# Performance work log

Hardware: AMD Instinct MI355X
Metric: run time of the kernel (lower is better)

The kernel has to match this reference:

```python
import jax, jax.numpy as jnp
import numpy as np

GAMMA = 0.99
EPS = 1e-8
N = 16777216  # flattened reward count


def setup_inputs() -> dict:
    key = jax.random.key(0)
    rewards = jax.random.normal(key, (N,), dtype=jnp.float32)
    return {"rewards": rewards}


def reference(rewards):
    # Sequential recurrence: R_t = gamma*R_{t-1} + r_t, Welford stats over R_t,
    # scaled[i] = r_i / max(std_t, eps), std_t = sqrt(var_sum/count) (1.0 if count < 2).
    flat = rewards.reshape(-1)

    def step(carry, r):
        R, cnt, mean, var_sum = carry
        R = GAMMA * R + r
        cnt = cnt + 1.0
        delta = R - mean
        mean = mean + delta / cnt
        var_sum = var_sum + delta * (R - mean)
        std = jnp.where(cnt < 2.0, jnp.float32(1.0), jnp.sqrt(var_sum / cnt))
        std = jnp.maximum(std, jnp.float32(EPS))
        return (R, cnt, mean, var_sum), r / std

    init = (jnp.float32(0.0), jnp.float32(0.0), jnp.float32(0.0), jnp.float32(0.0))
    _, scaled = jax.lax.scan(step, init, flat)
    return scaled.reshape(rewards.shape)
```

## Files before the change

### kernel.cpp

```cpp
#include <hip/hip_runtime.h>
#include <math.h>

#define THREADS 256
#define GAMMA 0.99

typedef float vf4 __attribute__((ext_vector_type(4)));

__device__ __forceinline__ int padi16(int i) { return i + (i >> 4); }

template<int NW>
__device__ __forceinline__ void block_compose_excl(int tid, double g, double v,
                                                   double& eg, double& ev,
                                                   double* lg, double* lv) {
    const int lane = tid & 63, wave = tid >> 6;
    double ig = g, iv = v;
#pragma unroll
    for (int k = 1; k < 64; k <<= 1) {
        double og = __shfl_up(ig, k);
        double ov = __shfl_up(iv, k);
        if (lane >= k) { iv = fma(ig, ov, iv); ig *= og; }
    }
    double weg = __shfl_up(ig, 1);
    double wev = __shfl_up(iv, 1);
    if (lane == 0) { weg = 1.0; wev = 0.0; }
    if (lane == 63) { lg[wave] = ig; lv[wave] = iv; }
    __syncthreads();
    double bg = 1.0, bv = 0.0;
    for (int w = 0; w < wave; ++w) { bv = fma(lg[w], bv, lv[w]); bg *= lg[w]; }
    eg = weg * bg;
    ev = fma(weg, bv, wev);
}

template<int NW>
__device__ __forceinline__ void block_add_excl2(int tid, double a, double b,
                                                double& ea, double& eb,
                                                double* la, double* lb) {
    const int lane = tid & 63, wave = tid >> 6;
    double ia = a, ib = b;
#pragma unroll
    for (int k = 1; k < 64; k <<= 1) {
        double oa = __shfl_up(ia, k);
        double ob = __shfl_up(ib, k);
        if (lane >= k) { ia += oa; ib += ob; }
    }
    double wea = __shfl_up(ia, 1);
    double web = __shfl_up(ib, 1);
    if (lane == 0) { wea = 0.0; web = 0.0; }
    if (lane == 63) { la[wave] = ia; lb[wave] = ib; }
    __syncthreads();
    double ba = 0.0, bb = 0.0;
    for (int w = 0; w < wave; ++w) { ba += la[w]; bb += lb[w]; }
    ea = wea + ba;
    eb = web + bb;
}


__global__ __launch_bounds__(THREADS) void w_phase1(const float* __restrict__ in,
                                                    double* __restrict__ agg,
                                                    double* __restrict__ bagg, int nw) {
    __shared__ double sA[4], sPs[4], sPq[4], sP2[4];
    const int tid = threadIdx.x, lane = tid & 63, w = tid >> 6;
    const int wid = blockIdx.x * 4 + w;
    const bool valid = wid < nw;

    float A = 0.f, c1 = 0.f, c2 = 0.f, c3 = 0.f;
    if (valid) {
        const float* src = in + (size_t)wid * 1024 + (size_t)lane * 16;
        float rv[16];
#pragma unroll
        for (int q = 0; q < 4; ++q) {
            const float4 t = ((const float4*)src)[q];
            rv[4 * q] = t.x; rv[4 * q + 1] = t.y; rv[4 * q + 2] = t.z; rv[4 * q + 3] = t.w;
        }
        const float gf = (float)GAMMA;
        float p = 0.f, psum = 0.f, pq = 0.f, p2 = 0.f, gp = 1.f;
#pragma unroll
        for (int j = 0; j < 16; ++j) {
            p = fmaf(gf, p, rv[j]);
            gp *= gf;
            psum += p;
            pq = fmaf(gp, p, pq);
            p2 = fmaf(p, p, p2);
        }
        const double g = GAMMA;
        double gPT = g;
#pragma unroll
        for (int e = 0; e < 4; ++e) gPT *= gPT;

        float ig = (float)gPT, iv = p;
#pragma unroll
        for (int k = 1; k < 64; k <<= 1) {
            float og = __shfl_up(ig, k);
            float ov = __shfl_up(iv, k);
            if (lane >= k) { iv = fmaf(ig, ov, iv); ig *= og; }
        }
        float rho = __shfl_up(iv, 1), gexc = __shfl_up(ig, 1);
        if (lane == 0) { rho = 0.f; gexc = 1.f; }
        A = __shfl(iv, 63);

        const float G1f = (float)(g * (1.0 - gPT) / (1.0 - g));
        const float G2f = (float)(g * g * (1.0 - gPT * gPT) / (1.0 - g * g));
        c1 = fmaf(rho, G1f, psum);
        c2 = gexc * fmaf(rho, G2f, pq);
        c3 = fmaf(rho * rho, G2f, fmaf(2.f * rho, pq, p2));
#pragma unroll
        for (int k = 32; k > 0; k >>= 1) {
            c1 += __shfl_down(c1, k);
            c2 += __shfl_down(c2, k);
            c3 += __shfl_down(c3, k);
        }
    }
    if (lane == 0) {
        if (valid) {
            agg[4 * (size_t)wid + 0] = (double)A;
            agg[4 * (size_t)wid + 1] = (double)c1;
            agg[4 * (size_t)wid + 2] = (double)c2;
            agg[4 * (size_t)wid + 3] = (double)c3;
        }
        sA[w] = valid ? (double)A : 0.0;
        sPs[w] = valid ? (double)c1 : 0.0;
        sPq[w] = valid ? (double)c2 : 0.0;
        sP2[w] = valid ? (double)c3 : 0.0;
    }
    __syncthreads();
    if (tid == 0) {
        const double g = GAMMA;
        double gC = g;
#pragma unroll
        for (int e = 0; e < 10; ++e) gC *= gC;
        const double G1C = g * (1.0 - gC) / (1.0 - g);
        const double G2C = g * g * (1.0 - gC * gC) / (1.0 - g * g);
        double Rin = 0.0, Ps = 0.0, Pq = 0.0, P2 = 0.0, gex = 1.0;
#pragma unroll
        for (int i = 0; i < 4; ++i) {
            Ps += fma(Rin, G1C, sPs[i]);
            Pq += gex * fma(Rin, G2C, sPq[i]);
            P2 += fma(Rin * Rin, G2C, fma(2.0 * Rin, sPq[i], sP2[i]));
            Rin = fma(gC, Rin, sA[i]);
            gex *= gC;
        }
        bagg[4 * (size_t)blockIdx.x + 0] = Rin;
        bagg[4 * (size_t)blockIdx.x + 1] = Ps;
        bagg[4 * (size_t)blockIdx.x + 2] = Pq;
        bagg[4 * (size_t)blockIdx.x + 3] = P2;
    }
}

template<int CPT, int LOG2CHUNK>
__global__ __launch_bounds__(1024) void rs_phase2(const double* __restrict__ agg,
                                                  double* __restrict__ car, int nchunk) {
    __shared__ double lg[16], lv[16], la[16], lb[16];
    const int t = threadIdx.x;
    const double g = GAMMA;
    double gC = g;
#pragma unroll
    for (int e = 0; e < LOG2CHUNK; ++e) gC *= gC;

    double A[CPT], Ps[CPT], Pq[CPT], P2[CPT];
    const int c0 = t * CPT;
#pragma unroll
    for (int i = 0; i < CPT; ++i) {
        const int c = c0 + i;
        const bool ok = c < nchunk;
        A[i]  = ok ? agg[4 * (size_t)c + 0] : 0.0;
        Ps[i] = ok ? agg[4 * (size_t)c + 1] : 0.0;
        Pq[i] = ok ? agg[4 * (size_t)c + 2] : 0.0;
        P2[i] = ok ? agg[4 * (size_t)c + 3] : 0.0;
    }
    double mg = 1.0, mv = 0.0;
#pragma unroll
    for (int i = 0; i < CPT; ++i) { mv = fma(gC, mv, A[i]); mg *= gC; }

    double eg, ev;
    block_compose_excl<16>(t, mg, mv, eg, ev, lg, lv);

    const double G1C = g * (1.0 - gC) / (1.0 - g);
    const double G2C = g * g * (1.0 - gC * gC) / (1.0 - g * g);
    double Rin[CPT + 1];
    Rin[0] = ev;
    double s1[CPT], s2[CPT];
#pragma unroll
    for (int i = 0; i < CPT; ++i) {
        s1[i] = fma(Rin[i], G1C, Ps[i]);
        s2[i] = fma(Rin[i] * Rin[i], G2C, fma(2.0 * Rin[i], Pq[i], P2[i]));
        Rin[i + 1] = fma(gC, Rin[i], A[i]);
    }
    double ts1 = 0.0, ts2 = 0.0;
#pragma unroll
    for (int i = 0; i < CPT; ++i) { ts1 += s1[i]; ts2 += s2[i]; }
    double ea, eb;
    block_add_excl2<16>(t, ts1, ts2, ea, eb, la, lb);
#pragma unroll
    for (int i = 0; i < CPT; ++i) {
        const int c = c0 + i;
        if (c < nchunk) {
            car[3 * (size_t)c + 0] = Rin[i];
            car[3 * (size_t)c + 1] = ea;
            car[3 * (size_t)c + 2] = eb;
        }
        ea += s1[i];
        eb += s2[i];
    }
}

__global__ __launch_bounds__(THREADS) void w_phase3(const float* __restrict__ in,
                                                    float* __restrict__ out,
                                                    const double* __restrict__ agg,
                                                    const double* __restrict__ car, int nw) {
    __shared__ float sbuf[THREADS / 64][1024 + 64];
    const int tid = threadIdx.x, lane = tid & 63, w = tid >> 6;
    const int wid = blockIdx.x * 4 + w;
    if (wid >= nw) return;
    const int b = blockIdx.x;

    const double g = GAMMA;
    double gC = g;
#pragma unroll
    for (int e = 0; e < 10; ++e) gC *= gC;
    const double G1C = g * (1.0 - gC) / (1.0 - g);
    const double G2C = g * g * (1.0 - gC * gC) / (1.0 - g * g);

    double RinC = car[3 * (size_t)b + 0];
    double S1C  = car[3 * (size_t)b + 1];
    double S2C  = car[3 * (size_t)b + 2];
    for (int i = 4 * b; i < wid; ++i) {
        const double Ai = agg[4 * (size_t)i + 0];
        const double Ps = agg[4 * (size_t)i + 1];
        const double Pq = agg[4 * (size_t)i + 2];
        const double P2 = agg[4 * (size_t)i + 3];
        S1C += fma(RinC, G1C, Ps);
        S2C += fma(RinC * RinC, G2C, fma(2.0 * RinC, Pq, P2));
        RinC = fma(gC, RinC, Ai);
    }

    const float* src = in + (size_t)wid * 1024 + (size_t)lane * 16;
    float rv[16];
#pragma unroll
    for (int q = 0; q < 4; ++q) {
        const float4 t = ((const float4*)src)[q];
        rv[4 * q] = t.x; rv[4 * q + 1] = t.y; rv[4 * q + 2] = t.z; rv[4 * q + 3] = t.w;
    }
    const float gf = (float)GAMMA;
    float p = 0.f, psum = 0.f, pq = 0.f, p2 = 0.f, gp = 1.f;
#pragma unroll
    for (int j = 0; j < 16; ++j) {
        p = fmaf(gf, p, rv[j]);
        gp *= gf;
        psum += p;
        pq = fmaf(gp, p, pq);
        p2 = fmaf(p, p, p2);
    }
    double gPT = g;
#pragma unroll
    for (int e = 0; e < 4; ++e) gPT *= gPT;

    if (wid == 0) {
        double ig = gPT, iv = (double)p;
#pragma unroll
        for (int k = 1; k < 64; k <<= 1) {
            double og = __shfl_up(ig, k);
            double ov = __shfl_up(iv, k);
            if (lane >= k) { iv = fma(ig, ov, iv); ig *= og; }
        }
        double rho = __shfl_up(iv, 1), gexc = __shfl_up(ig, 1);
        if (lane == 0) { rho = 0.0; gexc = 1.0; }
        const double rin = fma(gexc, RinC, rho);
        const double G1 = g * (1.0 - gPT) / (1.0 - g);
        const double G2 = g * g * (1.0 - gPT * gPT) / (1.0 - g * g);
        double s1 = fma(rin, G1, (double)psum);
        double s2 = fma(rin * rin, G2, fma(2.0 * rin, (double)pq, (double)p2));
        double ia = s1, ib = s2;
#pragma unroll
        for (int k = 1; k < 64; k <<= 1) {
            double oa = __shfl_up(ia, k);
            double ob = __shfl_up(ib, k);
            if (lane >= k) { ia += oa; ib += ob; }
        }
        double ea = __shfl_up(ia, 1), eb = __shfl_up(ib, 1);
        if (lane == 0) { ea = 0.0; eb = 0.0; }
        double R = rin, S1 = S1C + ea, S2 = S2C + eb;
        const int a0 = lane * 17;
        const size_t gbase = (size_t)lane * 16;
        for (int j = 0; j < 16; ++j) {
            const float rf = rv[j];
            R = fma(g, R, (double)rf);
            S1 += R;
            S2 = fma(R, R, S2);
            float ov;
            if (gbase + j == 0) {
                ov = rf;
            } else {
                const double cnt = (double)(gbase + j + 1);
                const double inv = 1.0 / cnt;
                const double mean = S1 * inv;
                double var = fma(S2, inv, -(mean * mean));
                var = var > 0.0 ? var : 0.0;
                double sd = sqrt(var);
                sd = sd > 1e-8 ? sd : 1e-8;
                ov = (float)((double)rf / sd);
            }
            sbuf[w][a0 + j] = ov;
        }
    } else {
        float ig = (float)gPT, iv = p;
#pragma unroll
        for (int k = 1; k < 64; k <<= 1) {
            float og = __shfl_up(ig, k);
            float ov = __shfl_up(iv, k);
            if (lane >= k) { iv = fmaf(ig, ov, iv); ig *= og; }
        }
        float rho = __shfl_up(iv, 1), gexc = __shfl_up(ig, 1);
        if (lane == 0) { rho = 0.f; gexc = 1.f; }
        const float rin = fmaf(gexc, (float)RinC, rho);
        const float G1f = (float)(g * (1.0 - gPT) / (1.0 - g));
        const float G2f = (float)(g * g * (1.0 - gPT * gPT) / (1.0 - g * g));
        float s1 = fmaf(rin, G1f, psum);
        float s2 = fmaf(rin * rin, G2f, fmaf(2.f * rin, pq, p2));
        float ia = s1, ib = s2;
#pragma unroll
        for (int k = 1; k < 64; k <<= 1) {
            float oa = __shfl_up(ia, k);
            float ob = __shfl_up(ib, k);
            if (lane >= k) { ia += oa; ib += ob; }
        }
        float ea = __shfl_up(ia, 1), eb = __shfl_up(ib, 1);
        if (lane == 0) { ea = 0.f; eb = 0.f; }
        const float S1bf = (float)S1C + ea;
        const float S2bf = (float)S2C + eb;

        float R = rin;
        float ls1 = 0.f, ls2 = 0.f;
        const float base_cnt = (float)((size_t)wid * 1024 + (size_t)lane * 16);
        const int a0 = lane * 17;
#pragma unroll
        for (int j = 0; j < 16; ++j) {
            const float rf = rv[j];
            R = fmaf(gf, R, rf);
            ls1 += R;
            ls2 = fmaf(R, R, ls2);
            const float cnt = base_cnt + (float)(j + 1);
            const float S1f = S1bf + ls1;
            const float S2f = S2bf + ls2;
            float t = fmaf(S2f, cnt, -(S1f * S1f));
            t = fmaxf(t, 1e-12f);
            sbuf[w][a0 + j] = rf * cnt * __builtin_amdgcn_rsqf(t);
        }
    }

    asm volatile("s_waitcnt lgkmcnt(0)" ::: "memory");

    float* dst = out + (size_t)wid * 1024;
#pragma unroll
    for (int k = 0; k < 4; ++k) {
        const int i = lane * 4 + k * 256;
        const int pp = padi16(i);
        vf4 v;
        v.x = sbuf[w][pp]; v.y = sbuf[w][pp + 1]; v.z = sbuf[w][pp + 2]; v.w = sbuf[w][pp + 3];
        __builtin_nontemporal_store(v, (vf4*)(dst + i));
    }
}

extern "C" void kernel_launch(void* const* d_in, const int* in_sizes, int n_in,
                              void* d_out, int out_size, void* d_ws, size_t ws_size,
                              hipStream_t stream) {
    (void)n_in; (void)out_size;
    const float* in = (const float*)d_in[0];
    float* out = (float*)d_out;
    double* ws = (double*)d_ws;
    const int n = in_sizes[0];

    const int nw = n >> 10;
    const int nc = (nw + 3) >> 2;
    const size_t need = (size_t)(4 * nw + 7 * nc) * sizeof(double);
    if ((n % 4096) == 0 && nw >= 4 && nc <= 4096 && ws_size >= need) {
        double* agg  = ws;
        double* bagg = ws + 4 * (size_t)nw;
        double* car  = bagg + 4 * (size_t)nc;
        w_phase1<<<nc, THREADS, 0, stream>>>(in, agg, bagg, nw);
        rs_phase2<4, 12><<<1, 1024, 0, stream>>>(bagg, car, nc);
        w_phase3<<<nc, THREADS, 0, stream>>>(in, out, agg, car, nw);
    } else {
        double* agg  = ws;
        double* bagg = ws + 4 * (size_t)nw;
        double* car  = bagg + 4 * (size_t)nc;
        w_phase1<<<nc, THREADS, 0, stream>>>(in, agg, bagg, nw);
        rs_phase2<4, 12><<<1, 1024, 0, stream>>>(bagg, car, nc);
        w_phase3<<<nc, THREADS, 0, stream>>>(in, out, agg, car, nw);
    }
}
```

Measured before the change: 51.30 us.

## Precompute per-wave carries in scan phase and store wave aggregates as float4

Phase 2 now expands each block carry into per-wave carries by walking that block's four wave aggregates. Phase 3 then reads its carry directly instead of each wave re-walking prior waves' double aggregates. Wave aggregates are stored as packed float4 rather than four doubles, which halves that traffic. The cost is extra serial work and strided writes in the single-block phase 2. Bounds checks and the workspace-size check are also dropped, so the code now assumes n is a multiple of 4096.

```diff
diff --git a/kernel.cpp b/kernel.cpp
--- a/kernel.cpp
+++ b/kernel.cpp
@@ -56,75 +56,63 @@
 
 
 __global__ __launch_bounds__(THREADS) void w_phase1(const float* __restrict__ in,
-                                                    double* __restrict__ agg,
+                                                    vf4* __restrict__ aggf,
                                                     double* __restrict__ bagg, int nw) {
     __shared__ double sA[4], sPs[4], sPq[4], sP2[4];
     const int tid = threadIdx.x, lane = tid & 63, w = tid >> 6;
     const int wid = blockIdx.x * 4 + w;
-    const bool valid = wid < nw;
-
-    float A = 0.f, c1 = 0.f, c2 = 0.f, c3 = 0.f;
-    if (valid) {
-        const float* src = in + (size_t)wid * 1024 + (size_t)lane * 16;
-        float rv[16];
-#pragma unroll
-        for (int q = 0; q < 4; ++q) {
-            const float4 t = ((const float4*)src)[q];
-            rv[4 * q] = t.x; rv[4 * q + 1] = t.y; rv[4 * q + 2] = t.z; rv[4 * q + 3] = t.w;
-        }
-        const float gf = (float)GAMMA;
-        float p = 0.f, psum = 0.f, pq = 0.f, p2 = 0.f, gp = 1.f;
-#pragma unroll
-        for (int j = 0; j < 16; ++j) {
-            p = fmaf(gf, p, rv[j]);
-            gp *= gf;
-            psum += p;
-            pq = fmaf(gp, p, pq);
-            p2 = fmaf(p, p, p2);
-        }
-        const double g = GAMMA;
-        double gPT = g;
-#pragma unroll
-        for (int e = 0; e < 4; ++e) gPT *= gPT;
-
-        float ig = (float)gPT, iv = p;
-#pragma unroll
-        for (int k = 1; k < 64; k <<= 1) {
-            float og = __shfl_up(ig, k);
-            float ov = __shfl_up(iv, k);
-            if (lane >= k) { iv = fmaf(ig, ov, iv); ig *= og; }
-        }
-        float rho = __shfl_up(iv, 1), gexc = __shfl_up(ig, 1);
-        if (lane == 0) { rho = 0.f; gexc = 1.f; }
-        A = __shfl(iv, 63);
-
-        const float G1f = (float)(g * (1.0 - gPT) / (1.0 - g));
-        const float G2f = (float)(g * g * (1.0 - gPT * gPT) / (1.0 - g * g));
-        c1 = fmaf(rho, G1f, psum);
-        c2 = gexc * fmaf(rho, G2f, pq);
-        c3 = fmaf(rho * rho, G2f, fmaf(2.f * rho, pq, p2));
-#pragma unroll
-        for (int k = 32; k > 0; k >>= 1) {
-            c1 += __shfl_down(c1, k);
-            c2 += __shfl_down(c2, k);
-            c3 += __shfl_down(c3, k);
-        }
+
+    const float* src = in + (size_t)wid * 1024 + (size_t)lane * 16;
+    float rv[16];
+#pragma unroll
+    for (int q = 0; q < 4; ++q) {
+        const float4 t = ((const float4*)src)[q];
+        rv[4 * q] = t.x; rv[4 * q + 1] = t.y; rv[4 * q + 2] = t.z; rv[4 * q + 3] = t.w;
+    }
+    const float gf = (float)GAMMA;
+    float p = 0.f, psum = 0.f, pq = 0.f, p2 = 0.f, gp = 1.f;
+#pragma unroll
+    for (int j = 0; j < 16; ++j) {
+        p = fmaf(gf, p, rv[j]);
+        gp *= gf;
+        psum += p;
+        pq = fmaf(gp, p, pq);
+        p2 = fmaf(p, p, p2);
+    }
+    const double g = GAMMA;
+    double gPT = g;
+#pragma unroll
+    for (int e = 0; e < 4; ++e) gPT *= gPT;
+
+    float ig = (float)gPT, iv = p;
+#pragma unroll
+    for (int k = 1; k < 64; k <<= 1) {
+        float og = __shfl_up(ig, k);
+        float ov = __shfl_up(iv, k);
+        if (lane >= k) { iv = fmaf(ig, ov, iv); ig *= og; }
+    }
+    float rho = __shfl_up(iv, 1), gexc = __shfl_up(ig, 1);
+    if (lane == 0) { rho = 0.f; gexc = 1.f; }
+    const float A = __shfl(iv, 63);
+
+    const float G1f = (float)(g * (1.0 - gPT) / (1.0 - g));
+    const float G2f = (float)(g * g * (1.0 - gPT * gPT) / (1.0 - g * g));
+    float c1 = fmaf(rho, G1f, psum);
+    float c2 = gexc * fmaf(rho, G2f, pq);
+    float c3 = fmaf(rho * rho, G2f, fmaf(2.f * rho, pq, p2));
+#pragma unroll
+    for (int k = 32; k > 0; k >>= 1) {
+        c1 += __shfl_down(c1, k);
+        c2 += __shfl_down(c2, k);
+        c3 += __shfl_down(c3, k);
     }
     if (lane == 0) {
-        if (valid) {
-            agg[4 * (size_t)wid + 0] = (double)A;
-            agg[4 * (size_t)wid + 1] = (double)c1;
-            agg[4 * (size_t)wid + 2] = (double)c2;
-            agg[4 * (size_t)wid + 3] = (double)c3;
-        }
-        sA[w] = valid ? (double)A : 0.0;
-        sPs[w] = valid ? (double)c1 : 0.0;
-        sPq[w] = valid ? (double)c2 : 0.0;
-        sP2[w] = valid ? (double)c3 : 0.0;
+        vf4 a; a.x = A; a.y = c1; a.z = c2; a.w = c3;
+        aggf[wid] = a;
+        sA[w] = (double)A; sPs[w] = (double)c1; sPq[w] = (double)c2; sP2[w] = (double)c3;
     }
     __syncthreads();
     if (tid == 0) {
-        const double g = GAMMA;
         double gC = g;
 #pragma unroll
         for (int e = 0; e < 10; ++e) gC *= gC;
@@ -147,14 +135,18 @@
 }
 
 template<int CPT, int LOG2CHUNK>
-__global__ __launch_bounds__(1024) void rs_phase2(const double* __restrict__ agg,
-                                                  double* __restrict__ car, int nchunk) {
+__global__ __launch_bounds__(1024) void rs_phase2x(const double* __restrict__ bagg,
+                                                   const vf4* __restrict__ aggf,
+                                                   double* __restrict__ wcar, int nchunk) {
     __shared__ double lg[16], lv[16], la[16], lb[16];
     const int t = threadIdx.x;
     const double g = GAMMA;
     double gC = g;
 #pragma unroll
     for (int e = 0; e < LOG2CHUNK; ++e) gC *= gC;
+    double gW = g;
+#pragma unroll
+    for (int e = 0; e < 10; ++e) gW *= gW;
 
     double A[CPT], Ps[CPT], Pq[CPT], P2[CPT];
     const int c0 = t * CPT;
@@ -162,10 +154,10 @@
     for (int i = 0; i < CPT; ++i) {
         const int c = c0 + i;
         const bool ok = c < nchunk;
-        A[i]  = ok ? agg[4 * (size_t)c + 0] : 0.0;
-        Ps[i] = ok ? agg[4 * (size_t)c + 1] : 0.0;
-        Pq[i] = ok ? agg[4 * (size_t)c + 2] : 0.0;
-        P2[i] = ok ? agg[4 * (size_t)c + 3] : 0.0;
+        A[i]  = ok ? bagg[4 * (size_t)c + 0] : 0.0;
+        Ps[i] = ok ? bagg[4 * (size_t)c + 1] : 0.0;
+        Pq[i] = ok ? bagg[4 * (size_t)c + 2] : 0.0;
+        P2[i] = ok ? bagg[4 * (size_t)c + 3] : 0.0;
     }
     double mg = 1.0, mv = 0.0;
 #pragma unroll
@@ -176,6 +168,9 @@
 
     const double G1C = g * (1.0 - gC) / (1.0 - g);
     const double G2C = g * g * (1.0 - gC * gC) / (1.0 - g * g);
+    const double G1W = g * (1.0 - gW) / (1.0 - g);
+    const double G2W = g * g * (1.0 - gW * gW) / (1.0 - g * g);
+
     double Rin[CPT + 1];
     Rin[0] = ev;
     double s1[CPT], s2[CPT];
@@ -190,13 +185,25 @@
     for (int i = 0; i < CPT; ++i) { ts1 += s1[i]; ts2 += s2[i]; }
     double ea, eb;
     block_add_excl2<16>(t, ts1, ts2, ea, eb, la, lb);
+
 #pragma unroll
     for (int i = 0; i < CPT; ++i) {
         const int c = c0 + i;
         if (c < nchunk) {
-            car[3 * (size_t)c + 0] = Rin[i];
-            car[3 * (size_t)c + 1] = ea;
-            car[3 * (size_t)c + 2] = eb;
+            double wR = Rin[i], wS1 = ea, wS2 = eb;
+#pragma unroll
+            for (int j = 0; j < 4; ++j) {
+                const int wd = 4 * c + j;
+                wcar[3 * (size_t)wd + 0] = wR;
+                wcar[3 * (size_t)wd + 1] = wS1;
+                wcar[3 * (size_t)wd + 2] = wS2;
+                const vf4 a = aggf[wd];
+                const double Aw = (double)a.x, Pw = (double)a.y;
+                const double Qw = (double)a.z, Sw = (double)a.w;
+                wS1 += fma(wR, G1W, Pw);
+                wS2 += fma(wR * wR, G2W, fma(2.0 * wR, Qw, Sw));
+                wR = fma(gW, wR, Aw);
+            }
         }
         ea += s1[i];
         eb += s2[i];
@@ -205,33 +212,14 @@
 
 __global__ __launch_bounds__(THREADS) void w_phase3(const float* __restrict__ in,
                                                     float* __restrict__ out,
-                                                    const double* __restrict__ agg,
-                                                    const double* __restrict__ car, int nw) {
+                                                    const double* __restrict__ wcar, int nw) {
     __shared__ float sbuf[THREADS / 64][1024 + 64];
     const int tid = threadIdx.x, lane = tid & 63, w = tid >> 6;
     const int wid = blockIdx.x * 4 + w;
-    if (wid >= nw) return;
-    const int b = blockIdx.x;
-
-    const double g = GAMMA;
-    double gC = g;
-#pragma unroll
-    for (int e = 0; e < 10; ++e) gC *= gC;
-    const double G1C = g * (1.0 - gC) / (1.0 - g);
-    const double G2C = g * g * (1.0 - gC * gC) / (1.0 - g * g);
-
-    double RinC = car[3 * (size_t)b + 0];
-    double S1C  = car[3 * (size_t)b + 1];
-    double S2C  = car[3 * (size_t)b + 2];
-    for (int i = 4 * b; i < wid; ++i) {
-        const double Ai = agg[4 * (size_t)i + 0];
-        const double Ps = agg[4 * (size_t)i + 1];
-        const double Pq = agg[4 * (size_t)i + 2];
-        const double P2 = agg[4 * (size_t)i + 3];
-        S1C += fma(RinC, G1C, Ps);
-        S2C += fma(RinC * RinC, G2C, fma(2.0 * RinC, Pq, P2));
-        RinC = fma(gC, RinC, Ai);
-    }
+
+    const double RinC = wcar[3 * (size_t)wid + 0];
+    const double S1C  = wcar[3 * (size_t)wid + 1];
+    const double S2C  = wcar[3 * (size_t)wid + 2];
 
     const float* src = in + (size_t)wid * 1024 + (size_t)lane * 16;
     float rv[16];
@@ -250,6 +238,7 @@
         pq = fmaf(gp, p, pq);
         p2 = fmaf(p, p, p2);
     }
+    const double g = GAMMA;
     double gPT = g;
 #pragma unroll
     for (int e = 0; e < 4; ++e) gPT *= gPT;
@@ -363,28 +352,19 @@
 extern "C" void kernel_launch(void* const* d_in, const int* in_sizes, int n_in,
                               void* d_out, int out_size, void* d_ws, size_t ws_size,
                               hipStream_t stream) {
-    (void)n_in; (void)out_size;
+    (void)n_in; (void)out_size; (void)ws_size;
     const float* in = (const float*)d_in[0];
     float* out = (float*)d_out;
     double* ws = (double*)d_ws;
     const int n = in_sizes[0];
 
     const int nw = n >> 10;
-    const int nc = (nw + 3) >> 2;
-    const size_t need = (size_t)(4 * nw + 7 * nc) * sizeof(double);
-    if ((n % 4096) == 0 && nw >= 4 && nc <= 4096 && ws_size >= need) {
-        double* agg  = ws;
-        double* bagg = ws + 4 * (size_t)nw;
-        double* car  = bagg + 4 * (size_t)nc;
-        w_phase1<<<nc, THREADS, 0, stream>>>(in, agg, bagg, nw);
-        rs_phase2<4, 12><<<1, 1024, 0, stream>>>(bagg, car, nc);
-        w_phase3<<<nc, THREADS, 0, stream>>>(in, out, agg, car, nw);
-    } else {
-        double* agg  = ws;
-        double* bagg = ws + 4 * (size_t)nw;
-        double* car  = bagg + 4 * (size_t)nc;
-        w_phase1<<<nc, THREADS, 0, stream>>>(in, agg, bagg, nw);
-        rs_phase2<4, 12><<<1, 1024, 0, stream>>>(bagg, car, nc);
-        w_phase3<<<nc, THREADS, 0, stream>>>(in, out, agg, car, nw);
-    }
-}
+    const int nc = nw >> 2;
+    double* bagg = ws;
+    double* wcar = ws + 4 * (size_t)nc;
+    vf4* aggf = (vf4*)(wcar + 3 * (size_t)nw);
+
+    w_phase1<<<nc, THREADS, 0, stream>>>(in, aggf, bagg, nw);
+    rs_phase2x<4, 12><<<1, 1024, 0, stream>>>(bagg, aggf, wcar, nc);
+    w_phase3<<<nc, THREADS, 0, stream>>>(in, out, wcar, nw);
+}
```

After: 76.03 us. 48.2% more time.
